# Kernel tuning notes

Measured on AMD Instinct MI355X. Metric: run time of the kernel, lower is better.

## Reference

```python
import jax, jax.numpy as jnp
import numpy as np

N_STATE = 1024
N_HEAD = 16
HEAD_DIM = N_STATE // N_HEAD
SCALE = HEAD_DIM ** (-0.25)


def setup_inputs() -> dict:
    key = jax.random.key(0)
    ks = jax.random.split(key, 9)
    B, S, D = 32, 1500, N_STATE
    std = 1.0 / np.sqrt(D)
    return {
        "hidden_states": jax.random.normal(ks[0], (B, 1, D), dtype=jnp.float32),
        "encoder_output": jax.random.normal(ks[1], (B, S, D), dtype=jnp.float32),
        "Wq": jax.random.normal(ks[2], (D, D), dtype=jnp.float32) * std,
        "bq": jax.random.normal(ks[3], (D,), dtype=jnp.float32) * std,
        "Wk": jax.random.normal(ks[4], (D, D), dtype=jnp.float32) * std,
        "Wv": jax.random.normal(ks[5], (D, D), dtype=jnp.float32) * std,
        "bv": jax.random.normal(ks[6], (D,), dtype=jnp.float32) * std,
        "Wo": jax.random.normal(ks[7], (D, D), dtype=jnp.float32) * std,
        "bo": jax.random.normal(ks[8], (D,), dtype=jnp.float32) * std,
    }


def reference(hidden_states, encoder_output, Wq, bq, Wk, Wv, bv, Wo, bo):
    B = hidden_states.shape[0]
    S = encoder_output.shape[1]
    # projections (torch F.linear: x @ W.T + b)
    q = hidden_states @ Wq.T + bq                  # [B, 1, D]
    k_original = encoder_output @ Wk.T             # [B, S, D] (no bias)
    v_original = encoder_output @ Wv.T + bv        # [B, S, D]

    q = q.reshape(B, 1, N_HEAD, HEAD_DIM).transpose(0, 2, 1, 3)         # [B,H,1,hd]
    k = k_original.reshape(B, S, N_HEAD, HEAD_DIM).transpose(0, 2, 1, 3)  # [B,H,S,hd]
    v = v_original.reshape(B, S, N_HEAD, HEAD_DIM).transpose(0, 2, 1, 3)  # [B,H,S,hd]

    # pre-scaled q and k, scores in fp32 softmax then cast back
    attn_weights = jnp.einsum('bhqd,bhkd->bhqk', q * SCALE, k * SCALE)  # [B,H,1,S]
    attn_weights = jax.nn.softmax(attn_weights.astype(jnp.float32), axis=-1).astype(q.dtype)
    attn_output = jnp.einsum('bhqk,bhkd->bhqd', attn_weights, v)        # [B,H,1,hd]
    attn_output = attn_output.transpose(0, 2, 1, 3).reshape(B, 1, N_STATE)
    attn_output = attn_output @ Wo.T + bo
    return attn_output, k_original, v_original
```

## Files before the change

kernel.cpp:

```cpp
#include <hip/hip_runtime.h>
#include <cstdint>
#include <cstddef>

#define D_MODEL 1024
#define NH      16
#define HD      64
#define B_SZ    32
#define SEQ     1500
#define MROWS   (B_SZ * SEQ)
#define KD      1024
#define NCHUNK  4
#define CLEN    (SEQ / NCHUNK)

typedef __attribute__((ext_vector_type(8))) short bf16x8;
typedef __attribute__((ext_vector_type(4))) float f32x4;
typedef unsigned short u16;

__device__ __forceinline__ u16 f2b(float f) {
  unsigned int x = __float_as_uint(f);
  x = (x + 0x7FFFu + ((x >> 16) & 1u)) >> 16;
  return (u16)x;
}

#define CAST_BLOCKS 3072
#define QPROJ_BLOCKS 64

__global__ __launch_bounds__(256) void cast_all_q(const float* __restrict__ enc,
                                                  const float* __restrict__ Wk,
                                                  const float* __restrict__ Wv,
                                                  const float* __restrict__ hs,
                                                  const float* __restrict__ Wq,
                                                  const float* __restrict__ bq,
                                                  u16* __restrict__ encb,
                                                  u16* __restrict__ wkvb,
                                                  float* __restrict__ qs) {
  const int tid = threadIdx.x;
  if (blockIdx.x < CAST_BLOCKS) {
    const int NA = MROWS * KD / 8;
    const int NW = KD * KD / 8;
    int stride = CAST_BLOCKS * 256;
    for (int i = blockIdx.x * 256 + tid; i < NA + 2 * NW; i += stride) {
      const float* s; u16* d;
      if (i < NA)            { s = enc + (size_t)i * 8;            d = encb + (size_t)i * 8; }
      else if (i < NA + NW)  { size_t j = i - NA;      s = Wk + j * 8; d = wkvb + j * 8; }
      else                   { size_t j = i - NA - NW; s = Wv + j * 8; d = wkvb + (size_t)NW * 8 + j * 8; }
      const float4* s4 = reinterpret_cast<const float4*>(s);
      float4 a = s4[0], b = s4[1];
      u16 u[8];
      u[0]=f2b(a.x); u[1]=f2b(a.y); u[2]=f2b(a.z); u[3]=f2b(a.w);
      u[4]=f2b(b.x); u[5]=f2b(b.y); u[6]=f2b(b.z); u[7]=f2b(b.w);
      *reinterpret_cast<uint4*>(d) = *reinterpret_cast<const uint4*>(u);
    }
  } else {
    const int qb = blockIdx.x - CAST_BLOCKS;
    const int n  = qb * 16 + (tid & 15);
    const int bb = tid >> 4;
    const float4* wp  = (const float4*)(Wq + (size_t)n * D_MODEL);
    const float4* x0p = (const float4*)(hs + (size_t)bb * D_MODEL);
    const float4* x1p = (const float4*)(hs + (size_t)(bb + 16) * D_MODEL);
    float a0 = 0.f, a1 = 0.f;
    #pragma unroll 8
    for (int i = 0; i < D_MODEL / 4; ++i) {
      float4 w = wp[i], x0 = x0p[i], x1 = x1p[i];
      a0 += w.x * x0.x + w.y * x0.y + w.z * x0.z + w.w * x0.w;
      a1 += w.x * x1.x + w.y * x1.y + w.z * x1.z + w.w * x1.w;
    }
    const float bqn = bq[n];
    qs[(size_t)bb * D_MODEL + n]        = (a0 + bqn) * 0.125f;
    qs[(size_t)(bb + 16) * D_MODEL + n] = (a1 + bqn) * 0.125f;
  }
}

#define GBM 128
#define GBN 256
#define GBK 32
#define GNT (KD / GBK)

__device__ __forceinline__ void stageA(const u16* __restrict__ Ag, u16* lbuf,
                                       long m0, int kt, int tid) {
  int c = tid;
  int r = c >> 2, cp = c & 3;
  int scp = cp ^ ((r >> 1) & 3);
  const u16* src = Ag + (m0 + r) * (long)KD + kt * GBK + scp * 8;
  __builtin_amdgcn_global_load_lds((const __attribute__((address_space(1))) void*)src,
      (__attribute__((address_space(3))) void*)(lbuf + (size_t)c * 8), 16, 0, 0);
}

__device__ __forceinline__ void stageB(const u16* __restrict__ Bg, u16* lbuf,
                                       int n0, int kt, int tid) {
  #pragma unroll
  for (int L = 0; L < 2; ++L) {
    int c = tid + L * 512;
    int r = c >> 2, cp = c & 3;
    int scp = cp ^ ((r >> 1) & 3);
    const u16* src = Bg + (size_t)(n0 + r) * KD + kt * GBK + scp * 8;
    __builtin_amdgcn_global_load_lds((const __attribute__((address_space(1))) void*)src,
        (__attribute__((address_space(3))) void*)(lbuf + (size_t)c * 8), 16, 0, 0);
  }
}

__device__ __forceinline__ bf16x8 ldFrag(const u16* buf, int row, int lane) {
  int r  = row + (lane & 15);
  int ch = (lane >> 4) ^ ((r >> 1) & 3);
  return *(const bf16x8*)(buf + (size_t)r * GBK + ch * 8);
}

__global__ __launch_bounds__(512, 4) void gemm_kv(const u16* __restrict__ A,
                                                  const u16* __restrict__ Bm,
                                                  const float* __restrict__ bv,
                                                  float* __restrict__ Kout,
                                                  float* __restrict__ Vout) {
  __shared__ __align__(16) char smem[2 * (GBM + GBN) * GBK * 2];
  u16* sA0 = (u16*)smem;
  u16* sA1 = sA0 + GBM * GBK;
  u16* sB0 = sA1 + GBM * GBK;
  u16* sB1 = sB0 + GBN * GBK;

  const int tid  = threadIdx.x;
  const int lane = tid & 63;
  const int wid  = tid >> 6;
  const int wr   = wid >> 2;
  const int wc   = wid & 3;

  int bx = (blockIdx.x & 7) * (gridDim.x >> 3) + (blockIdx.x >> 3);
  const int  mt = bx >> 3;
  const int  nt = bx & 7;
  const long m0 = (long)mt * GBM;
  const int  n0 = nt * GBN;

  stageA(A, sA0, m0, 0, tid);
  stageB(Bm, sB0, n0, 0, tid);
  stageA(A, sA1, m0, 1, tid);
  stageB(Bm, sB1, n0, 1, tid);

  f32x4 acc[4][4] = {};

  for (int t = 0; t < GNT; ++t) {
    if (t == GNT - 1) { asm volatile("s_waitcnt vmcnt(0)" ::: "memory"); }
    else              { asm volatile("s_waitcnt vmcnt(3)" ::: "memory"); }
    __builtin_amdgcn_s_barrier();

    const u16* cA = (t & 1) ? sA1 : sA0;
    const u16* cB = (t & 1) ? sB1 : sB0;
    bf16x8 af[4], bfr[4];
    #pragma unroll
    for (int mf = 0; mf < 4; ++mf) af[mf]  = ldFrag(cA, wr * 64 + mf * 16, lane);
    #pragma unroll
    for (int nf = 0; nf < 4; ++nf) bfr[nf] = ldFrag(cB, wc * 64 + nf * 16, lane);
    asm volatile("s_waitcnt lgkmcnt(0)" ::: "memory");
    __builtin_amdgcn_s_barrier();

    if (t + 2 < GNT) {
      u16* pA = (t & 1) ? sA1 : sA0;
      u16* pB = (t & 1) ? sB1 : sB0;
      stageA(A, pA, m0, t + 2, tid);
      stageB(Bm, pB, n0, t + 2, tid);
    }

    #pragma unroll
    for (int mf = 0; mf < 4; ++mf)
      #pragma unroll
      for (int nf = 0; nf < 4; ++nf)
        acc[mf][nf] = __builtin_amdgcn_mfma_f32_16x16x32_bf16(af[mf], bfr[nf], acc[mf][nf], 0, 0, 0);
  }

  __syncthreads();
  float (*ep)[260] = (float(*)[260])smem;

  const bool isV = (nt >= 4);
  float* Co = isV ? Vout : Kout;
  const int ncol0 = isV ? (n0 - 1024) : n0;
  float4 bias4[4];
  #pragma unroll
  for (int k = 0; k < 4; ++k) {
    int c4 = (tid + 512 * k) & 63;
    bias4[k] = isV ? reinterpret_cast<const float4*>(bv)[(ncol0 >> 2) + c4]
                   : make_float4(0.f, 0.f, 0.f, 0.f);
  }

  #pragma unroll
  for (int p = 0; p < 4; ++p) {
    if (wr == (p >> 1)) {
      const int mfb = (p & 1) * 2;
      #pragma unroll
      for (int mm = 0; mm < 2; ++mm)
        #pragma unroll
        for (int nf = 0; nf < 4; ++nf)
          #pragma unroll
          for (int r = 0; r < 4; ++r)
            ep[mm * 16 + (lane >> 4) * 4 + r][wc * 64 + nf * 16 + (lane & 15)] =
                acc[mfb + mm][nf][r];
    }
    __syncthreads();
    #pragma unroll
    for (int k = 0; k < 4; ++k) {
      int idx = tid + 512 * k;
      int row = idx >> 6;
      int c4  = idx & 63;
      long grow = m0 + p * 32 + row;
      float4 v = *reinterpret_cast<const float4*>(&ep[row][c4 * 4]);
      v.x += bias4[k].x; v.y += bias4[k].y; v.z += bias4[k].z; v.w += bias4[k].w;
      *reinterpret_cast<float4*>(&Co[grow * D_MODEL + ncol0 + c4 * 4]) = v;
    }
    __syncthreads();
  }
}

__global__ __launch_bounds__(256) void attn_part(const float* __restrict__ qs,
                                                 const float* __restrict__ K,
                                                 const float* __restrict__ V,
                                                 float* __restrict__ part) {
  const int blk = blockIdx.x;
  const int bh = blk >> 2, c = blk & 3;
  const int b = bh >> 4, h = bh & 15;
  const int tid = threadIdx.x;
  const int s0 = c * CLEN;

  __shared__ float sc[CLEN];
  __shared__ float red[256];
  __shared__ float pvs[16][HD];

  const int j  = tid & 15;
  const int rg = tid >> 4;
  const float4 q4 = *(const float4*)(qs + (size_t)b * D_MODEL + h * HD + j * 4);
  float lmax = -1e30f;
  for (int i = rg; i < CLEN; i += 16) {
    const float4 k4 = *(const float4*)(K + (size_t)(b * SEQ + s0 + i) * D_MODEL + h * HD + j * 4);
    float p = q4.x * k4.x + q4.y * k4.y + q4.z * k4.z + q4.w * k4.w;
    p += __shfl_xor(p, 1);
    p += __shfl_xor(p, 2);
    p += __shfl_xor(p, 4);
    p += __shfl_xor(p, 8);
    if (j == 0) sc[i] = p;
    lmax = fmaxf(lmax, p);
  }
  red[tid] = lmax; __syncthreads();
  for (int off = 128; off; off >>= 1) {
    if (tid < off) red[tid] = fmaxf(red[tid], red[tid + off]);
    __syncthreads();
  }
  const float m = red[0]; __syncthreads();

  float lsum = 0.f;
  for (int i = tid; i < CLEN; i += 256) {
    float p = __expf(sc[i] - m);
    sc[i] = p;
    lsum += p;
  }
  red[tid] = lsum; __syncthreads();
  for (int off = 128; off; off >>= 1) {
    if (tid < off) red[tid] += red[tid + off];
    __syncthreads();
  }
  const float l = red[0];

  const int dq = tid & 15;
  const int sg = tid >> 4;
  float4 a4 = make_float4(0.f, 0.f, 0.f, 0.f);
  for (int i = sg; i < CLEN; i += 16) {
    float p = sc[i];
    float4 v4 = *(const float4*)(V + (size_t)(b * SEQ + s0 + i) * D_MODEL + h * HD + dq * 4);
    a4.x += p * v4.x; a4.y += p * v4.y; a4.z += p * v4.z; a4.w += p * v4.w;
  }
  *(float4*)&pvs[sg][dq * 4] = a4;
  __syncthreads();

  if (tid < HD) {
    float a = 0.f;
    #pragma unroll
    for (int g = 0; g < 16; ++g) a += pvs[g][tid];
    float* pp = part + (size_t)blk * 66;
    pp[2 + tid] = a;
    if (tid == 0) { pp[0] = m; pp[1] = l; }
  }
}

__global__ __launch_bounds__(64) void attn_comb(const float* __restrict__ part,
                                                float* __restrict__ attnc) {
  const int bh = blockIdx.x;
  const int b = bh >> 4, h = bh & 15;
  const int tid = threadIdx.x;
  const float* pp = part + (size_t)bh * 4 * 66;
  const float m0 = pp[0], m1 = pp[66], m2 = pp[132], m3 = pp[198];
  const float M = fmaxf(fmaxf(m0, m1), fmaxf(m2, m3));
  const float w0 = __expf(m0 - M), w1 = __expf(m1 - M),
              w2 = __expf(m2 - M), w3 = __expf(m3 - M);
  const float L = pp[1] * w0 + pp[67] * w1 + pp[133] * w2 + pp[199] * w3;
  const float o = (pp[2 + tid] * w0 + pp[68 + tid] * w1 +
                   pp[134 + tid] * w2 + pp[200 + tid] * w3) / L;
  attnc[(size_t)b * D_MODEL + h * HD + tid] = o;
}

__global__ __launch_bounds__(256) void oproj_kernel(const float* __restrict__ x,
                                                    const float* __restrict__ Wo,
                                                    const float* __restrict__ bo,
                                                    float* __restrict__ out) {
  const int b = blockIdx.x >> 3, ch = blockIdx.x & 7;
  const int tid = threadIdx.x;
  __shared__ float xs[D_MODEL];
  ((float4*)xs)[tid] = ((const float4*)(x + (size_t)b * D_MODEL))[tid];
  __syncthreads();
  const int n = ch * 128 + (tid >> 1);
  const int half = tid & 1;
  const float4* wp = (const float4*)(Wo + (size_t)n * D_MODEL + half * 512);
  const float4* xp = (const float4*)xs + half * 128;
  float a = 0.f;
  #pragma unroll 8
  for (int i = 0; i < 128; ++i) {
    float4 w = wp[i], xv = xp[i];
    a += w.x * xv.x + w.y * xv.y + w.z * xv.z + w.w * xv.w;
  }
  a += __shfl_xor(a, 1);
  if (!half) out[(size_t)b * D_MODEL + n] = a + bo[n];
}

extern "C" void kernel_launch(void* const* d_in, const int* in_sizes, int n_in,
                              void* d_out, int out_size, void* d_ws, size_t ws_size,
                              hipStream_t stream) {
  const float* hs  = (const float*)d_in[0];
  const float* enc = (const float*)d_in[1];
  const float* Wq  = (const float*)d_in[2];
  const float* bq  = (const float*)d_in[3];
  const float* Wk  = (const float*)d_in[4];
  const float* Wv  = (const float*)d_in[5];
  const float* bv  = (const float*)d_in[6];
  const float* Wo  = (const float*)d_in[7];
  const float* bo  = (const float*)d_in[8];

  float* out   = (float*)d_out;
  float* attnO = out;
  float* Kout  = out + 32768;
  float* Vout  = Kout + (size_t)MROWS * D_MODEL;

  char* ws = (char*)d_ws;
  const size_t off_wkvb  = (size_t)MROWS * D_MODEL * 2;
  const size_t off_qs    = off_wkvb + 4194304;
  const size_t off_attnc = off_qs + 131072;
  const size_t off_part  = off_attnc + 131072;

  u16*   encb  = (u16*)ws;
  u16*   wkvb  = (u16*)(ws + off_wkvb);
  float* qs    = (float*)(ws + off_qs);
  float* attnc = (float*)(ws + off_attnc);
  float* part  = (float*)(ws + off_part);

  cast_all_q<<<CAST_BLOCKS + QPROJ_BLOCKS, 256, 0, stream>>>(enc, Wk, Wv, hs, Wq, bq,
                                                             encb, wkvb, qs);

  gemm_kv<<<(MROWS / GBM) * (2048 / GBN), 512, 0, stream>>>(encb, wkvb, bv, Kout, Vout);

  attn_part<<<B_SZ * NH * NCHUNK, 256, 0, stream>>>(qs, Kout, Vout, part);
  attn_comb<<<B_SZ * NH, 64, 0, stream>>>(part, attnc);
  oproj_kernel<<<B_SZ * 8, 256, 0, stream>>>(attnc, Wo, bo, attnO);
}
```

Baseline: 457.1 us.

## Fuse encoder fp32-to-bf16 cast into GEMM A staging and merge combine into oproj

Removes the standalone cast pass over the encoder output by loading fp32 A tiles into registers, converting them with packed bf16 conversion, and writing them to LDS. A three-deep prefetch hides the latency. The attention-combine step is folded into the output projection kernel, dropping one launch and an intermediate buffer. The trade-off is that the GEMM now reads fp32 A, doubling its A-side global/L2 traffic, and uses more registers and a register-staged load path instead of direct-to-LDS loads.

```diff
diff --git a/kernel.cpp b/kernel.cpp
--- a/kernel.cpp
+++ b/kernel.cpp
@@ -22,28 +22,31 @@
   return (u16)x;
 }
 
-#define CAST_BLOCKS 3072
+__device__ __forceinline__ unsigned cvtpk(float lo, float hi) {
+  unsigned r;
+  asm("v_cvt_pk_bf16_f32 %0, %1, %2" : "=v"(r) : "v"(lo), "v"(hi));
+  return r;
+}
+
+#define SCHED_FENCE() asm volatile("" ::: "memory")
+
+#define WCAST_BLOCKS 256
 #define QPROJ_BLOCKS 64
 
-__global__ __launch_bounds__(256) void cast_all_q(const float* __restrict__ enc,
-                                                  const float* __restrict__ Wk,
-                                                  const float* __restrict__ Wv,
-                                                  const float* __restrict__ hs,
-                                                  const float* __restrict__ Wq,
-                                                  const float* __restrict__ bq,
-                                                  u16* __restrict__ encb,
-                                                  u16* __restrict__ wkvb,
-                                                  float* __restrict__ qs) {
+__global__ __launch_bounds__(256) void prep_kernel(const float* __restrict__ Wk,
+                                                   const float* __restrict__ Wv,
+                                                   const float* __restrict__ hs,
+                                                   const float* __restrict__ Wq,
+                                                   const float* __restrict__ bq,
+                                                   u16* __restrict__ wkvb,
+                                                   float* __restrict__ qs) {
   const int tid = threadIdx.x;
-  if (blockIdx.x < CAST_BLOCKS) {
-    const int NA = MROWS * KD / 8;
+  if (blockIdx.x < WCAST_BLOCKS) {
     const int NW = KD * KD / 8;
-    int stride = CAST_BLOCKS * 256;
-    for (int i = blockIdx.x * 256 + tid; i < NA + 2 * NW; i += stride) {
-      const float* s; u16* d;
-      if (i < NA)            { s = enc + (size_t)i * 8;            d = encb + (size_t)i * 8; }
-      else if (i < NA + NW)  { size_t j = i - NA;      s = Wk + j * 8; d = wkvb + j * 8; }
-      else                   { size_t j = i - NA - NW; s = Wv + j * 8; d = wkvb + (size_t)NW * 8 + j * 8; }
+    int stride = WCAST_BLOCKS * 256;
+    for (int i = blockIdx.x * 256 + tid; i < 2 * NW; i += stride) {
+      const float* s = (i < NW) ? (Wk + (size_t)i * 8) : (Wv + (size_t)(i - NW) * 8);
+      u16* d = wkvb + (size_t)i * 8;
       const float4* s4 = reinterpret_cast<const float4*>(s);
       float4 a = s4[0], b = s4[1];
       u16 u[8];
@@ -52,7 +55,7 @@
       *reinterpret_cast<uint4*>(d) = *reinterpret_cast<const uint4*>(u);
     }
   } else {
-    const int qb = blockIdx.x - CAST_BLOCKS;
+    const int qb = blockIdx.x - WCAST_BLOCKS;
     const int n  = qb * 16 + (tid & 15);
     const int bb = tid >> 4;
     const float4* wp  = (const float4*)(Wq + (size_t)n * D_MODEL);
@@ -76,14 +79,22 @@
 #define GBK 32
 #define GNT (KD / GBK)
 
-__device__ __forceinline__ void stageA(const u16* __restrict__ Ag, u16* lbuf,
-                                       long m0, int kt, int tid) {
-  int c = tid;
-  int r = c >> 2, cp = c & 3;
+__device__ __forceinline__ void loadA(const float* __restrict__ Ag, long m0, int kt,
+                                      int tid, float4& x0, float4& x1) {
+  int r = tid >> 2, cp = tid & 3;
   int scp = cp ^ ((r >> 1) & 3);
-  const u16* src = Ag + (m0 + r) * (long)KD + kt * GBK + scp * 8;
-  __builtin_amdgcn_global_load_lds((const __attribute__((address_space(1))) void*)src,
-      (__attribute__((address_space(3))) void*)(lbuf + (size_t)c * 8), 16, 0, 0);
+  const float* src = Ag + (m0 + r) * (long)KD + kt * GBK + scp * 8;
+  x0 = *reinterpret_cast<const float4*>(src);
+  x1 = *reinterpret_cast<const float4*>(src + 4);
+}
+
+__device__ __forceinline__ void writeA(u16* lbuf, int tid, float4 x0, float4 x1) {
+  uint4 p;
+  p.x = cvtpk(x0.x, x0.y);
+  p.y = cvtpk(x0.z, x0.w);
+  p.z = cvtpk(x1.x, x1.y);
+  p.w = cvtpk(x1.z, x1.w);
+  *reinterpret_cast<uint4*>(lbuf + (size_t)tid * 8) = p;
 }
 
 __device__ __forceinline__ void stageB(const u16* __restrict__ Bg, u16* lbuf,
@@ -105,7 +116,7 @@
   return *(const bf16x8*)(buf + (size_t)r * GBK + ch * 8);
 }
 
-__global__ __launch_bounds__(512, 4) void gemm_kv(const u16* __restrict__ A,
+__global__ __launch_bounds__(512, 4) void gemm_kv(const float* __restrict__ A,
                                                   const u16* __restrict__ Bm,
                                                   const float* __restrict__ bv,
                                                   float* __restrict__ Kout,
@@ -128,16 +139,26 @@
   const long m0 = (long)mt * GBM;
   const int  n0 = nt * GBN;
 
-  stageA(A, sA0, m0, 0, tid);
+  float4 p00, p01, p10, p11, aw0, aw1, al0, al1;
+  loadA(A, m0, 0, tid, p00, p01);
+  loadA(A, m0, 1, tid, p10, p11);
+  SCHED_FENCE();
   stageB(Bm, sB0, n0, 0, tid);
-  stageA(A, sA1, m0, 1, tid);
+  SCHED_FENCE();
+  loadA(A, m0, 2, tid, aw0, aw1);
+  SCHED_FENCE();
   stageB(Bm, sB1, n0, 1, tid);
+  SCHED_FENCE();
+  writeA(sA0, tid, p00, p01);
+  writeA(sA1, tid, p10, p11);
+  asm volatile("s_waitcnt lgkmcnt(0)" ::: "memory");
 
   f32x4 acc[4][4] = {};
 
   for (int t = 0; t < GNT; ++t) {
-    if (t == GNT - 1) { asm volatile("s_waitcnt vmcnt(0)" ::: "memory"); }
-    else              { asm volatile("s_waitcnt vmcnt(3)" ::: "memory"); }
+    if (t <= GNT - 3)      { asm volatile("s_waitcnt vmcnt(4)" ::: "memory"); }
+    else if (t == GNT - 2) { asm volatile("s_waitcnt vmcnt(2)" ::: "memory"); }
+    else                   { asm volatile("s_waitcnt vmcnt(0)" ::: "memory"); }
     __builtin_amdgcn_s_barrier();
 
     const u16* cA = (t & 1) ? sA1 : sA0;
@@ -147,15 +168,19 @@
     for (int mf = 0; mf < 4; ++mf) af[mf]  = ldFrag(cA, wr * 64 + mf * 16, lane);
     #pragma unroll
     for (int nf = 0; nf < 4; ++nf) bfr[nf] = ldFrag(cB, wc * 64 + nf * 16, lane);
+
+    if (t + 3 < GNT) loadA(A, m0, t + 3, tid, al0, al1);
+
     asm volatile("s_waitcnt lgkmcnt(0)" ::: "memory");
     __builtin_amdgcn_s_barrier();
 
     if (t + 2 < GNT) {
       u16* pA = (t & 1) ? sA1 : sA0;
       u16* pB = (t & 1) ? sB1 : sB0;
-      stageA(A, pA, m0, t + 2, tid);
+      writeA(pA, tid, aw0, aw1);
       stageB(Bm, pB, n0, t + 2, tid);
     }
+    aw0 = al0; aw1 = al1;
 
     #pragma unroll
     for (int mf = 0; mf < 4; ++mf)
@@ -275,31 +300,33 @@
   }
 }
 
-__global__ __launch_bounds__(64) void attn_comb(const float* __restrict__ part,
-                                                float* __restrict__ attnc) {
-  const int bh = blockIdx.x;
-  const int b = bh >> 4, h = bh & 15;
-  const int tid = threadIdx.x;
-  const float* pp = part + (size_t)bh * 4 * 66;
-  const float m0 = pp[0], m1 = pp[66], m2 = pp[132], m3 = pp[198];
-  const float M = fmaxf(fmaxf(m0, m1), fmaxf(m2, m3));
-  const float w0 = __expf(m0 - M), w1 = __expf(m1 - M),
-              w2 = __expf(m2 - M), w3 = __expf(m3 - M);
-  const float L = pp[1] * w0 + pp[67] * w1 + pp[133] * w2 + pp[199] * w3;
-  const float o = (pp[2 + tid] * w0 + pp[68 + tid] * w1 +
-                   pp[134 + tid] * w2 + pp[200 + tid] * w3) / L;
-  attnc[(size_t)b * D_MODEL + h * HD + tid] = o;
-}
-
-__global__ __launch_bounds__(256) void oproj_kernel(const float* __restrict__ x,
-                                                    const float* __restrict__ Wo,
-                                                    const float* __restrict__ bo,
-                                                    float* __restrict__ out) {
+__global__ __launch_bounds__(256) void oproj_comb(const float* __restrict__ part,
+                                                  const float* __restrict__ Wo,
+                                                  const float* __restrict__ bo,
+                                                  float* __restrict__ out) {
   const int b = blockIdx.x >> 3, ch = blockIdx.x & 7;
   const int tid = threadIdx.x;
   __shared__ float xs[D_MODEL];
-  ((float4*)xs)[tid] = ((const float4*)(x + (size_t)b * D_MODEL))[tid];
+
+  {
+    const int h = tid >> 4;
+    const int d = (tid & 15) * 4;
+    const float* pp = part + (size_t)(b * NH + h) * 4 * 66;
+    const float m0 = pp[0], l0 = pp[1], m1 = pp[66], l1 = pp[67],
+                m2 = pp[132], l2 = pp[133], m3 = pp[198], l3 = pp[199];
+    const float M = fmaxf(fmaxf(m0, m1), fmaxf(m2, m3));
+    const float w0 = __expf(m0 - M), w1 = __expf(m1 - M),
+                w2 = __expf(m2 - M), w3 = __expf(m3 - M);
+    const float inv = 1.0f / (l0 * w0 + l1 * w1 + l2 * w2 + l3 * w3);
+    #pragma unroll
+    for (int jj = 0; jj < 4; ++jj) {
+      float o = pp[2 + d + jj] * w0 + pp[68 + d + jj] * w1 +
+                pp[134 + d + jj] * w2 + pp[200 + d + jj] * w3;
+      xs[h * HD + d + jj] = o * inv;
+    }
+  }
   __syncthreads();
+
   const int n = ch * 128 + (tid >> 1);
   const int half = tid & 1;
   const float4* wp = (const float4*)(Wo + (size_t)n * D_MODEL + half * 512);
@@ -333,23 +360,14 @@
   float* Vout  = Kout + (size_t)MROWS * D_MODEL;
 
   char* ws = (char*)d_ws;
-  const size_t off_wkvb  = (size_t)MROWS * D_MODEL * 2;
-  const size_t off_qs    = off_wkvb + 4194304;
-  const size_t off_attnc = off_qs + 131072;
-  const size_t off_part  = off_attnc + 131072;
-
-  u16*   encb  = (u16*)ws;
-  u16*   wkvb  = (u16*)(ws + off_wkvb);
-  float* qs    = (float*)(ws + off_qs);
-  float* attnc = (float*)(ws + off_attnc);
-  float* part  = (float*)(ws + off_part);
-
-  cast_all_q<<<CAST_BLOCKS + QPROJ_BLOCKS, 256, 0, stream>>>(enc, Wk, Wv, hs, Wq, bq,
-                                                             encb, wkvb, qs);
-
-  gemm_kv<<<(MROWS / GBM) * (2048 / GBN), 512, 0, stream>>>(encb, wkvb, bv, Kout, Vout);
+  u16*   wkvb = (u16*)ws;
+  float* qs   = (float*)(ws + 4194304);
+  float* part = (float*)(ws + 4194304 + 131072);
+
+  prep_kernel<<<WCAST_BLOCKS + QPROJ_BLOCKS, 256, 0, stream>>>(Wk, Wv, hs, Wq, bq, wkvb, qs);
+
+  gemm_kv<<<(MROWS / GBM) * (2048 / GBN), 512, 0, stream>>>(enc, wkvb, bv, Kout, Vout);
 
   attn_part<<<B_SZ * NH * NCHUNK, 256, 0, stream>>>(qs, Kout, Vout, part);
-  attn_comb<<<B_SZ * NH, 64, 0, stream>>>(part, attnc);
-  oproj_kernel<<<B_SZ * 8, 256, 0, stream>>>(attnc, Wo, bo, attnO);
-}
+  oproj_comb<<<B_SZ * 8, 256, 0, stream>>>(part, Wo, bo, attnO);
+}
```

Result: slower. 481.5 us (+5.3%).

## Split attention into per-wavefront chunks and fuse softmax combine into output projection

Applied to the files above, without the earlier changes.

Each wavefront in attn_part now owns its own sequence chunk (16 chunks per head instead of 4 per block). Reductions use wave shuffles instead of shared-memory trees with block barriers. The separate combine kernel is removed, and the log-sum-exp merge of the 16 partials moves into the output-projection kernel's prologue. This removes many __syncthreads and one kernel launch. In exchange, each of the 8 oproj blocks per batch redundantly recombines that batch's partials.

```diff
diff --git a/kernel.cpp b/kernel.cpp
--- a/kernel.cpp
+++ b/kernel.cpp
@@ -9,8 +9,8 @@
 #define SEQ     1500
 #define MROWS   (B_SZ * SEQ)
 #define KD      1024
-#define NCHUNK  4
-#define CLEN    (SEQ / NCHUNK)
+#define NCH     16
+#define PSTR    68
 
 typedef __attribute__((ext_vector_type(8))) short bf16x8;
 typedef __attribute__((ext_vector_type(4))) float f32x4;
@@ -211,20 +211,23 @@
                                                  const float* __restrict__ V,
                                                  float* __restrict__ part) {
   const int blk = blockIdx.x;
-  const int bh = blk >> 2, c = blk & 3;
+  const int bh = blk >> 2, qb = blk & 3;
   const int b = bh >> 4, h = bh & 15;
-  const int tid = threadIdx.x;
-  const int s0 = c * CLEN;
-
-  __shared__ float sc[CLEN];
-  __shared__ float red[256];
-  __shared__ float pvs[16][HD];
-
-  const int j  = tid & 15;
-  const int rg = tid >> 4;
+  const int w = threadIdx.x >> 6;
+  const int lane = threadIdx.x & 63;
+  const int c = qb * 4 + w;
+  const int s0 = (c * SEQ) >> 4;
+  const int L = (((c + 1) * SEQ) >> 4) - s0;
+
+  __shared__ float scs[4][96];
+  float* sc = scs[w];
+
+  const int j  = lane & 15;
+  const int rg = lane >> 4;
   const float4 q4 = *(const float4*)(qs + (size_t)b * D_MODEL + h * HD + j * 4);
+
   float lmax = -1e30f;
-  for (int i = rg; i < CLEN; i += 16) {
+  for (int i = rg; i < L; i += 4) {
     const float4 k4 = *(const float4*)(K + (size_t)(b * SEQ + s0 + i) * D_MODEL + h * HD + j * 4);
     float p = q4.x * k4.x + q4.y * k4.y + q4.z * k4.z + q4.w * k4.w;
     p += __shfl_xor(p, 1);
@@ -234,72 +237,73 @@
     if (j == 0) sc[i] = p;
     lmax = fmaxf(lmax, p);
   }
-  red[tid] = lmax; __syncthreads();
-  for (int off = 128; off; off >>= 1) {
-    if (tid < off) red[tid] = fmaxf(red[tid], red[tid + off]);
-    __syncthreads();
-  }
-  const float m = red[0]; __syncthreads();
+  lmax = fmaxf(lmax, __shfl_xor(lmax, 16));
+  lmax = fmaxf(lmax, __shfl_xor(lmax, 32));
+  const float m = lmax;
+  asm volatile("s_waitcnt lgkmcnt(0)" ::: "memory");
 
   float lsum = 0.f;
-  for (int i = tid; i < CLEN; i += 256) {
+  for (int i = lane; i < L; i += 64) {
     float p = __expf(sc[i] - m);
     sc[i] = p;
     lsum += p;
   }
-  red[tid] = lsum; __syncthreads();
-  for (int off = 128; off; off >>= 1) {
-    if (tid < off) red[tid] += red[tid + off];
-    __syncthreads();
-  }
-  const float l = red[0];
-
-  const int dq = tid & 15;
-  const int sg = tid >> 4;
+  lsum += __shfl_xor(lsum, 1);
+  lsum += __shfl_xor(lsum, 2);
+  lsum += __shfl_xor(lsum, 4);
+  lsum += __shfl_xor(lsum, 8);
+  lsum += __shfl_xor(lsum, 16);
+  lsum += __shfl_xor(lsum, 32);
+  asm volatile("s_waitcnt lgkmcnt(0)" ::: "memory");
+
   float4 a4 = make_float4(0.f, 0.f, 0.f, 0.f);
-  for (int i = sg; i < CLEN; i += 16) {
+  for (int i = rg; i < L; i += 4) {
     float p = sc[i];
-    float4 v4 = *(const float4*)(V + (size_t)(b * SEQ + s0 + i) * D_MODEL + h * HD + dq * 4);
+    float4 v4 = *(const float4*)(V + (size_t)(b * SEQ + s0 + i) * D_MODEL + h * HD + j * 4);
     a4.x += p * v4.x; a4.y += p * v4.y; a4.z += p * v4.z; a4.w += p * v4.w;
   }
-  *(float4*)&pvs[sg][dq * 4] = a4;
-  __syncthreads();
-
-  if (tid < HD) {
-    float a = 0.f;
-    #pragma unroll
-    for (int g = 0; g < 16; ++g) a += pvs[g][tid];
-    float* pp = part + (size_t)blk * 66;
-    pp[2 + tid] = a;
-    if (tid == 0) { pp[0] = m; pp[1] = l; }
-  }
-}
-
-__global__ __launch_bounds__(64) void attn_comb(const float* __restrict__ part,
-                                                float* __restrict__ attnc) {
-  const int bh = blockIdx.x;
-  const int b = bh >> 4, h = bh & 15;
-  const int tid = threadIdx.x;
-  const float* pp = part + (size_t)bh * 4 * 66;
-  const float m0 = pp[0], m1 = pp[66], m2 = pp[132], m3 = pp[198];
-  const float M = fmaxf(fmaxf(m0, m1), fmaxf(m2, m3));
-  const float w0 = __expf(m0 - M), w1 = __expf(m1 - M),
-              w2 = __expf(m2 - M), w3 = __expf(m3 - M);
-  const float L = pp[1] * w0 + pp[67] * w1 + pp[133] * w2 + pp[199] * w3;
-  const float o = (pp[2 + tid] * w0 + pp[68 + tid] * w1 +
-                   pp[134 + tid] * w2 + pp[200 + tid] * w3) / L;
-  attnc[(size_t)b * D_MODEL + h * HD + tid] = o;
-}
-
-__global__ __launch_bounds__(256) void oproj_kernel(const float* __restrict__ x,
-                                                    const float* __restrict__ Wo,
-                                                    const float* __restrict__ bo,
-                                                    float* __restrict__ out) {
+  a4.x += __shfl_xor(a4.x, 16); a4.x += __shfl_xor(a4.x, 32);
+  a4.y += __shfl_xor(a4.y, 16); a4.y += __shfl_xor(a4.y, 32);
+  a4.z += __shfl_xor(a4.z, 16); a4.z += __shfl_xor(a4.z, 32);
+  a4.w += __shfl_xor(a4.w, 16); a4.w += __shfl_xor(a4.w, 32);
+
+  float* pp = part + (size_t)(bh * NCH + c) * PSTR;
+  if (lane < 16) *(float4*)(pp + lane * 4) = a4;
+  if (lane == 0) { pp[64] = m; pp[65] = lsum; }
+}
+
+__global__ __launch_bounds__(256) void oproj_comb(const float* __restrict__ part,
+                                                  const float* __restrict__ Wo,
+                                                  const float* __restrict__ bo,
+                                                  float* __restrict__ out) {
   const int b = blockIdx.x >> 3, ch = blockIdx.x & 7;
   const int tid = threadIdx.x;
   __shared__ float xs[D_MODEL];
-  ((float4*)xs)[tid] = ((const float4*)(x + (size_t)b * D_MODEL))[tid];
+
+  {
+    const int h = tid >> 4;
+    const int d = (tid & 15) * 4;
+    const float* pp = part + (size_t)(b * NH + h) * NCH * PSTR;
+    float M = -1e30f;
+    #pragma unroll
+    for (int cc = 0; cc < NCH; ++cc) M = fmaxf(M, pp[cc * PSTR + 64]);
+    float Lsum = 0.f;
+    float4 o = make_float4(0.f, 0.f, 0.f, 0.f);
+    #pragma unroll
+    for (int cc = 0; cc < NCH; ++cc) {
+      const float wgt = __expf(pp[cc * PSTR + 64] - M);
+      Lsum += pp[cc * PSTR + 65] * wgt;
+      float4 pv = *(const float4*)(pp + cc * PSTR + d);
+      o.x += pv.x * wgt; o.y += pv.y * wgt; o.z += pv.z * wgt; o.w += pv.w * wgt;
+    }
+    const float inv = 1.0f / Lsum;
+    xs[h * HD + d]     = o.x * inv;
+    xs[h * HD + d + 1] = o.y * inv;
+    xs[h * HD + d + 2] = o.z * inv;
+    xs[h * HD + d + 3] = o.w * inv;
+  }
   __syncthreads();
+
   const int n = ch * 128 + (tid >> 1);
   const int half = tid & 1;
   const float4* wp = (const float4*)(Wo + (size_t)n * D_MODEL + half * 512);
@@ -333,23 +337,20 @@
   float* Vout  = Kout + (size_t)MROWS * D_MODEL;
 
   char* ws = (char*)d_ws;
-  const size_t off_wkvb  = (size_t)MROWS * D_MODEL * 2;
-  const size_t off_qs    = off_wkvb + 4194304;
-  const size_t off_attnc = off_qs + 131072;
-  const size_t off_part  = off_attnc + 131072;
-
-  u16*   encb  = (u16*)ws;
-  u16*   wkvb  = (u16*)(ws + off_wkvb);
-  float* qs    = (float*)(ws + off_qs);
-  float* attnc = (float*)(ws + off_attnc);
-  float* part  = (float*)(ws + off_part);
+  const size_t off_wkvb = (size_t)MROWS * D_MODEL * 2;
+  const size_t off_qs   = off_wkvb + 4194304;
+  const size_t off_part = off_qs + 131072;
+
+  u16*   encb = (u16*)ws;
+  u16*   wkvb = (u16*)(ws + off_wkvb);
+  float* qs   = (float*)(ws + off_qs);
+  float* part = (float*)(ws + off_part);
 
   cast_all_q<<<CAST_BLOCKS + QPROJ_BLOCKS, 256, 0, stream>>>(enc, Wk, Wv, hs, Wq, bq,
                                                              encb, wkvb, qs);
 
   gemm_kv<<<(MROWS / GBM) * (2048 / GBN), 512, 0, stream>>>(encb, wkvb, bv, Kout, Vout);
 
-  attn_part<<<B_SZ * NH * NCHUNK, 256, 0, stream>>>(qs, Kout, Vout, part);
-  attn_comb<<<B_SZ * NH, 64, 0, stream>>>(part, attnc);
-  oproj_kernel<<<B_SZ * 8, 256, 0, stream>>>(attnc, Wo, bo, attnO);
-}
+  attn_part<<<B_SZ * NH * 4, 256, 0, stream>>>(qs, Kout, Vout, part);
+  oproj_comb<<<B_SZ * 8, 256, 0, stream>>>(part, Wo, bo, attnO);
+}
```

Result: no change. 458.4 us (+0.3%).
